# Kernel optimization log

Hardware: AMD Instinct MI355X
Metric: run time of the kernel (lower is better)

## Reference

```python
import jax, jax.numpy as jnp
import numpy as np

NUM_CODES = 100000
DIM = 64
N = 65536   # B*T flattened visits
L = 48      # max codes per visit (padded with -1)
C = 1.0     # Poincare ball curvature
MIN_NORM = 1e-15
BALL_EPS = 1e-5   # geoopt projx boundary eps for float32
ATANH_EPS = 1e-7  # clamp artanh argument below 1


def _projx(x):
    # Poincare ball projection: pull points with norm >= (1-eps)/sqrt(c) back inside.
    sqrt_c = jnp.sqrt(C)
    norm = jnp.maximum(jnp.linalg.norm(x, axis=-1, keepdims=True), MIN_NORM)
    maxnorm = (1.0 - BALL_EPS) / sqrt_c
    return jnp.where(norm > maxnorm, x * (maxnorm / norm), x)


def setup_inputs() -> dict:
    key = jax.random.key(0)
    k1, k2, k3 = jax.random.split(key, 3)
    emb = jax.random.normal(k1, (NUM_CODES, DIM), dtype=jnp.float32) * 0.001
    emb = _projx(emb)
    ids = jax.random.randint(k2, (N, L), 0, NUM_CODES)
    pad = jax.random.uniform(k3, (N, L)) < 0.3
    code_ids = jnp.where(pad, jnp.int64(-1) if jax.config.jax_enable_x64 else -1, ids)
    return {"code_ids": code_ids, "emb": emb}


def reference(code_ids, emb):
    # code_ids: [N, L] int, -1 = padding; emb: [NUM_CODES, DIM] Poincare points.
    sqrt_c = jnp.sqrt(jnp.asarray(C, emb.dtype))
    mask = code_ids >= 0                               # [N, L]
    safe_ids = jnp.where(mask, code_ids, 0)
    x = emb[safe_ids]                                  # [N, L, D] gather
    # logmap0: artanh(sqrt(c)*||x||) * x / (sqrt(c)*||x||)
    norm = jnp.maximum(jnp.linalg.norm(x, axis=-1, keepdims=True), MIN_NORM)
    arg = jnp.minimum(sqrt_c * norm, 1.0 - ATANH_EPS)
    tangents = (jnp.arctanh(arg) / (sqrt_c * norm)) * x  # [N, L, D]
    m = mask[..., None].astype(emb.dtype)
    s = jnp.sum(tangents * m, axis=1)                  # [N, D]
    cnt = jnp.sum(m, axis=1)                           # [N, 1]
    return s / jnp.maximum(cnt, 1.0)                   # zeros for empty visits
```

## Files before the change

### kernel.cpp

```cpp
#include <hip/hip_runtime.h>


#define LCODES 48
#define DIM 64

__global__ __launch_bounds__(256)
void amax_kernel(const float* __restrict__ emb, unsigned* __restrict__ bmax,
                 long n4) {
    const uint4* __restrict__ u4 = reinterpret_cast<const uint4*>(emb);
    unsigned m = 0;
    for (long i = (long)blockIdx.x * 256 + threadIdx.x; i < n4; i += 256L * 256L) {
        const uint4 w = u4[i];
        m = max(m, w.x & 0x7fffffffu);
        m = max(m, w.y & 0x7fffffffu);
        m = max(m, w.z & 0x7fffffffu);
        m = max(m, w.w & 0x7fffffffu);
    }
    #pragma unroll
    for (int d = 1; d <= 32; d <<= 1)
        m = max(m, (unsigned)__shfl_xor((int)m, d, 64));
    __shared__ unsigned sm[4];
    if ((threadIdx.x & 63) == 0) sm[threadIdx.x >> 6] = m;
    __syncthreads();
    if (threadIdx.x == 0)
        bmax[blockIdx.x] = max(max(sm[0], sm[1]), max(sm[2], sm[3]));
}

__device__ __forceinline__ float global_amax256(const unsigned* __restrict__ bmax) {
    const int lane = threadIdx.x & 63;
    unsigned m = max(max(bmax[lane], bmax[lane + 64]),
                     max(bmax[lane + 128], bmax[lane + 192]));
    #pragma unroll
    for (int d = 1; d <= 32; d <<= 1)
        m = max(m, (unsigned)__shfl_xor((int)m, d, 64));
    return __uint_as_float(m);
}

__global__ __launch_bounds__(256)
void build_i8_kernel(const float* __restrict__ emb,
                     const unsigned* __restrict__ bmax,
                     unsigned char* __restrict__ tab,
                     float* __restrict__ qsout, int C) {
    const float amax = global_amax256(bmax);
    const float qs   = amax * (1.0006f / 127.f);
    const float invq = (amax > 0.f) ? (127.f / (amax * 1.0006f)) : 0.f;
    if (blockIdx.x == 0 && threadIdx.x == 0) qsout[0] = qs;

    const int tid  = threadIdx.x;
    const int lane = tid & 63;
    const int wave = tid >> 6;
    const int g = lane >> 3, s = lane & 7;
    const int r = blockIdx.x * 32 + wave * 8 + g;
    if (r >= C) return;

    const float4* __restrict__ emb4 = reinterpret_cast<const float4*>(emb);
    const float4 a = emb4[r * 16 + 2 * s];
    const float4 b = emb4[r * 16 + 2 * s + 1];

    float ss = a.x*a.x + a.y*a.y + a.z*a.z + a.w*a.w
             + b.x*b.x + b.y*b.y + b.z*b.z + b.w*b.w;
    ss += __shfl_xor(ss, 1, 64);
    ss += __shfl_xor(ss, 2, 64);
    ss += __shfl_xor(ss, 4, 64);

    float scale;
    if (__builtin_expect(ss > 0.04f, 0)) {
        const float norm = fmaxf(sqrtf(ss), 1e-15f);
        const float arg  = fminf(norm, 1.f - 1e-7f);
        scale = 0.5f * logf((1.f + arg) / (1.f - arg)) / norm;
    } else {
        scale = 1.f + ss * (0.33333333333f + ss * (0.2f + ss * 0.14285714285f));
    }
    scale *= invq;

    const float t[8] = { a.x*scale, a.y*scale, a.z*scale, a.w*scale,
                         b.x*scale, b.y*scale, b.z*scale, b.w*scale };
    unsigned u[8];
    #pragma unroll
    for (int k = 0; k < 8; ++k)
        u[k] = (unsigned)((int)rintf(t[k]) + 128);

    uint2 w;
    w.x = u[0] | (u[1] << 8) | (u[2] << 16) | (u[3] << 24);
    w.y = u[4] | (u[5] << 8) | (u[6] << 16) | (u[7] << 24);
    reinterpret_cast<uint2*>(tab)[r * 8 + s] = w;
}

__global__ __launch_bounds__(256)
void visit_gather_i8x2_kernel(const int* __restrict__ ids,
                              const unsigned char* __restrict__ tab,
                              const float* __restrict__ qsp,
                              float* __restrict__ out, int N) {
    const float qs = qsp[0];

    const int tid  = threadIdx.x;
    const int lane = tid & 63;
    const int wave = tid >> 6;
    const int v0   = (blockIdx.x * 4 + wave) * 2;
    if (v0 >= N) return;
    const bool has1 = (v0 + 1) < N;

    int myid0 = -1, myid1 = -1;
    if (lane < LCODES) {
        myid0 = ids[(long)v0 * LCODES + lane];
        if (has1) myid1 = ids[(long)(v0 + 1) * LCODES + lane];
    }

    const float cnt0 = (float)__popcll(__ballot(myid0 >= 0));
    const float cnt1 = (float)__popcll(__ballot(myid1 >= 0));

    const int g = lane >> 3;
    const int s = lane & 7;
    const uint2* __restrict__ tab2 = reinterpret_cast<const uint2*>(tab);

    unsigned aEx0 = 0, aOx0 = 0, aEy0 = 0, aOy0 = 0;
    unsigned aEx1 = 0, aOx1 = 0, aEy1 = 0, aOy1 = 0;

    #pragma unroll
    for (int it = 0; it < LCODES / 8; ++it) {
        const int j   = it * 8 + g;
        const int id0 = __shfl(myid0, j, 64);
        const int id1 = __shfl(myid1, j, 64);
        const unsigned msk0  = (id0 >= 0) ? 0xffffffffu : 0u;
        const unsigned msk1  = (id1 >= 0) ? 0xffffffffu : 0u;
        const unsigned base0 = ((unsigned)(id0 >= 0 ? id0 : 0)) << 3;
        const unsigned base1 = ((unsigned)(id1 >= 0 ? id1 : 0)) << 3;

        uint2 w0 = tab2[base0 + s];
        uint2 w1 = tab2[base1 + s];
        w0.x &= msk0;  w0.y &= msk0;
        w1.x &= msk1;  w1.y &= msk1;

        aEx0 +=  w0.x       & 0x00ff00ffu;
        aOx0 += (w0.x >> 8) & 0x00ff00ffu;
        aEy0 +=  w0.y       & 0x00ff00ffu;
        aOy0 += (w0.y >> 8) & 0x00ff00ffu;
        aEx1 +=  w1.x       & 0x00ff00ffu;
        aOx1 += (w1.x >> 8) & 0x00ff00ffu;
        aEy1 +=  w1.y       & 0x00ff00ffu;
        aOy1 += (w1.y >> 8) & 0x00ff00ffu;
    }

    #pragma unroll
    for (int d = 8; d <= 32; d <<= 1) {
        aEx0 += (unsigned)__shfl_xor((int)aEx0, d, 64);
        aOx0 += (unsigned)__shfl_xor((int)aOx0, d, 64);
        aEy0 += (unsigned)__shfl_xor((int)aEy0, d, 64);
        aOy0 += (unsigned)__shfl_xor((int)aOy0, d, 64);
        aEx1 += (unsigned)__shfl_xor((int)aEx1, d, 64);
        aOx1 += (unsigned)__shfl_xor((int)aOx1, d, 64);
        aEy1 += (unsigned)__shfl_xor((int)aEy1, d, 64);
        aOy1 += (unsigned)__shfl_xor((int)aOy1, d, 64);
    }

    if (lane < 16) {
        const bool second = lane >= 8;
        if (!second || has1) {
            const int  ss8   = lane & 7;
            const int  v     = v0 + (second ? 1 : 0);
            const float cnt  = second ? cnt1 : cnt0;
            const unsigned eX = second ? aEx1 : aEx0;
            const unsigned oX = second ? aOx1 : aOx0;
            const unsigned eY = second ? aEy1 : aEy0;
            const unsigned oY = second ? aOy1 : aOy0;

            const float qinv  = qs / fmaxf(cnt, 1.f);
            const float fbias = 128.f * cnt;
            float4 rA, rB;
            rA.x = ((float)(eX & 0xffffu) - fbias) * qinv;
            rA.y = ((float)(oX & 0xffffu) - fbias) * qinv;
            rA.z = ((float)(eX >> 16)     - fbias) * qinv;
            rA.w = ((float)(oX >> 16)     - fbias) * qinv;
            rB.x = ((float)(eY & 0xffffu) - fbias) * qinv;
            rB.y = ((float)(oY & 0xffffu) - fbias) * qinv;
            rB.z = ((float)(eY >> 16)     - fbias) * qinv;
            rB.w = ((float)(oY >> 16)     - fbias) * qinv;
            float4* o = reinterpret_cast<float4*>(out) + (long)v * (DIM / 4);
            o[2 * ss8]     = rA;
            o[2 * ss8 + 1] = rB;
        }
    }
}

__global__ __launch_bounds__(256, 4)
void visit_fp32_kernel(const int* __restrict__ ids,
                       const float* __restrict__ emb,
                       float* __restrict__ out, int N) {
    const int tid  = threadIdx.x;
    const int lane = tid & 63;
    const int wave = tid >> 6;
    const int v    = blockIdx.x * 4 + wave;
    if (v >= N) return;

    int myid = -1;
    if (lane < LCODES) myid = ids[(long)v * LCODES + lane];
    const unsigned long long valid = __ballot(myid >= 0);
    const float cnt = (float)__popcll(valid);
    const int g = lane >> 3, s = lane & 7;
    const float4* __restrict__ emb4 = reinterpret_cast<const float4*>(emb);
    float4 accA = make_float4(0.f,0.f,0.f,0.f), accB = make_float4(0.f,0.f,0.f,0.f);
    #pragma unroll
    for (int it = 0; it < LCODES / 8; ++it) {
        const int id = __shfl(myid, it * 8 + g, 64);
        const float keep = (id >= 0) ? 1.f : 0.f;
        const unsigned base = ((unsigned)(id >= 0 ? id : 0)) << 4;
        float4 a = emb4[base + s], b = emb4[base + 8 + s];
        float ss = a.x*a.x + a.y*a.y + a.z*a.z + a.w*a.w
                 + b.x*b.x + b.y*b.y + b.z*b.z + b.w*b.w;
        ss += __shfl_xor(ss, 1, 64);
        ss += __shfl_xor(ss, 2, 64);
        ss += __shfl_xor(ss, 4, 64);
        float scale;
        if (__builtin_expect(__any(ss > 0.04f), 0)) {
            const float norm = fmaxf(sqrtf(ss), 1e-15f);
            const float arg  = fminf(norm, 1.f - 1e-7f);
            scale = 0.5f * logf((1.f + arg) / (1.f - arg)) / norm;
        } else {
            scale = 1.f + ss * (0.33333333333f + ss * (0.2f + ss * 0.14285714285f));
        }
        scale *= keep;
        accA.x += a.x*scale; accA.y += a.y*scale; accA.z += a.z*scale; accA.w += a.w*scale;
        accB.x += b.x*scale; accB.y += b.y*scale; accB.z += b.z*scale; accB.w += b.w*scale;
    }
    #pragma unroll
    for (int d = 8; d <= 32; d <<= 1) {
        accA.x += __shfl_xor(accA.x, d, 64); accA.y += __shfl_xor(accA.y, d, 64);
        accA.z += __shfl_xor(accA.z, d, 64); accA.w += __shfl_xor(accA.w, d, 64);
        accB.x += __shfl_xor(accB.x, d, 64); accB.y += __shfl_xor(accB.y, d, 64);
        accB.z += __shfl_xor(accB.z, d, 64); accB.w += __shfl_xor(accB.w, d, 64);
    }
    if (lane < 8) {
        const float inv = 1.f / fmaxf(cnt, 1.f);
        float4* o = reinterpret_cast<float4*>(out) + (long)v * (DIM / 4);
        o[2*s]   = make_float4(accA.x*inv, accA.y*inv, accA.z*inv, accA.w*inv);
        o[2*s+1] = make_float4(accB.x*inv, accB.y*inv, accB.z*inv, accB.w*inv);
    }
}

extern "C" void kernel_launch(void* const* d_in, const int* in_sizes, int n_in,
                              void* d_out, int out_size, void* d_ws, size_t ws_size,
                              hipStream_t stream) {
    const int*   ids = (const int*)d_in[0];
    const float* emb = (const float*)d_in[1];
    float*       out = (float*)d_out;

    const int N = in_sizes[0] / LCODES;
    const int C = in_sizes[1] / DIM;

    const size_t tab_off = 4096;
    const size_t need = tab_off + (size_t)C * DIM;

    if (ws_size >= need) {
        unsigned*      bmax = (unsigned*)d_ws;
        float*         qsp  = (float*)((char*)d_ws + 1024);
        unsigned char* tab  = (unsigned char*)d_ws + tab_off;

        const long n4 = (long)C * DIM / 4;
        hipLaunchKernelGGL(amax_kernel, dim3(256), dim3(256), 0, stream,
                           emb, bmax, n4);
        const int blocksA = (C + 31) / 32;
        hipLaunchKernelGGL(build_i8_kernel, dim3(blocksA), dim3(256), 0, stream,
                           emb, bmax, tab, qsp, C);
        const int blocksB = (N + 7) / 8;
        hipLaunchKernelGGL(visit_gather_i8x2_kernel, dim3(blocksB), dim3(256), 0,
                           stream, ids, tab, qsp, out, N);
    } else {
        const int blocks = (N + 3) / 4;
        hipLaunchKernelGGL(visit_fp32_kernel, dim3(blocks), dim3(256), 0, stream,
                           ids, emb, out, N);
    }
}
```

Baseline: 108.3 us.

## Widen int8 gather to 16-byte loads with zero-row padding and wider amax grid

The visit gather kernel now reads each table row as four 16-byte loads per code instead of eight 8-byte loads, handling 16 codes per iteration across the wave. Padding ids point to an extra all-zero row appended to the table, which removes the per-load masking. Index loads and output stores are marked nontemporal. The amax pre-pass uses 1024 blocks with two loads per iteration. The aim is fewer, wider memory transactions and more parallelism in the pre-pass, at the cost of more accumulator registers and a longer shuffle reduction.

Measured after the change: 112.8 us. 1.04x slower.

```diff
diff --git a/kernel.cpp b/kernel.cpp
--- a/kernel.cpp
+++ b/kernel.cpp
@@ -3,18 +3,28 @@
 
 #define LCODES 48
 #define DIM 64
+
+typedef float vf4 __attribute__((ext_vector_type(4)));
 
 __global__ __launch_bounds__(256)
 void amax_kernel(const float* __restrict__ emb, unsigned* __restrict__ bmax,
                  long n4) {
     const uint4* __restrict__ u4 = reinterpret_cast<const uint4*>(emb);
+    const long T = (long)gridDim.x * 256;
     unsigned m = 0;
-    for (long i = (long)blockIdx.x * 256 + threadIdx.x; i < n4; i += 256L * 256L) {
-        const uint4 w = u4[i];
-        m = max(m, w.x & 0x7fffffffu);
-        m = max(m, w.y & 0x7fffffffu);
-        m = max(m, w.z & 0x7fffffffu);
-        m = max(m, w.w & 0x7fffffffu);
+    for (long i = (long)blockIdx.x * 256 + threadIdx.x; i < n4; i += 2 * T) {
+        const uint4 a = u4[i];
+        m = max(m, a.x & 0x7fffffffu);
+        m = max(m, a.y & 0x7fffffffu);
+        m = max(m, a.z & 0x7fffffffu);
+        m = max(m, a.w & 0x7fffffffu);
+        if (i + T < n4) {
+            const uint4 b = u4[i + T];
+            m = max(m, b.x & 0x7fffffffu);
+            m = max(m, b.y & 0x7fffffffu);
+            m = max(m, b.z & 0x7fffffffu);
+            m = max(m, b.w & 0x7fffffffu);
+        }
     }
     #pragma unroll
     for (int d = 1; d <= 32; d <<= 1)
@@ -26,10 +36,12 @@
         bmax[blockIdx.x] = max(max(sm[0], sm[1]), max(sm[2], sm[3]));
 }
 
-__device__ __forceinline__ float global_amax256(const unsigned* __restrict__ bmax) {
+__device__ __forceinline__ float global_amax1024(const unsigned* __restrict__ bmax) {
     const int lane = threadIdx.x & 63;
-    unsigned m = max(max(bmax[lane], bmax[lane + 64]),
-                     max(bmax[lane + 128], bmax[lane + 192]));
+    unsigned m = 0;
+    #pragma unroll
+    for (int k = 0; k < 16; ++k)
+        m = max(m, bmax[lane + 64 * k]);
     #pragma unroll
     for (int d = 1; d <= 32; d <<= 1)
         m = max(m, (unsigned)__shfl_xor((int)m, d, 64));
@@ -41,10 +53,12 @@
                      const unsigned* __restrict__ bmax,
                      unsigned char* __restrict__ tab,
                      float* __restrict__ qsout, int C) {
-    const float amax = global_amax256(bmax);
+    const float amax = global_amax1024(bmax);
     const float qs   = amax * (1.0006f / 127.f);
     const float invq = (amax > 0.f) ? (127.f / (amax * 1.0006f)) : 0.f;
     if (blockIdx.x == 0 && threadIdx.x == 0) qsout[0] = qs;
+    if (blockIdx.x == 0 && threadIdx.x < 16)
+        reinterpret_cast<unsigned*>(tab + (size_t)C * DIM)[threadIdx.x] = 0u;
 
     const int tid  = threadIdx.x;
     const int lane = tid & 63;
@@ -87,10 +101,10 @@
 }
 
 __global__ __launch_bounds__(256)
-void visit_gather_i8x2_kernel(const int* __restrict__ ids,
+void visit_gather_i8x4_kernel(const int* __restrict__ ids,
                               const unsigned char* __restrict__ tab,
                               const float* __restrict__ qsp,
-                              float* __restrict__ out, int N) {
+                              float* __restrict__ out, int N, int C) {
     const float qs = qsp[0];
 
     const int tid  = threadIdx.x;
@@ -102,82 +116,81 @@
 
     int myid0 = -1, myid1 = -1;
     if (lane < LCODES) {
-        myid0 = ids[(long)v0 * LCODES + lane];
-        if (has1) myid1 = ids[(long)(v0 + 1) * LCODES + lane];
+        myid0 = __builtin_nontemporal_load(&ids[(long)v0 * LCODES + lane]);
+        if (has1)
+            myid1 = __builtin_nontemporal_load(&ids[(long)(v0 + 1) * LCODES + lane]);
     }
 
     const float cnt0 = (float)__popcll(__ballot(myid0 >= 0));
     const float cnt1 = (float)__popcll(__ballot(myid1 >= 0));
 
-    const int g = lane >> 3;
-    const int s = lane & 7;
-    const uint2* __restrict__ tab2 = reinterpret_cast<const uint2*>(tab);
-
-    unsigned aEx0 = 0, aOx0 = 0, aEy0 = 0, aOy0 = 0;
-    unsigned aEx1 = 0, aOx1 = 0, aEy1 = 0, aOy1 = 0;
-
-    #pragma unroll
-    for (int it = 0; it < LCODES / 8; ++it) {
-        const int j   = it * 8 + g;
+    const int g = lane >> 2;
+    const int s = lane & 3;
+    const uint4* __restrict__ tab4 = reinterpret_cast<const uint4*>(tab);
+
+    unsigned aE0[4] = {0,0,0,0}, aO0[4] = {0,0,0,0};
+    unsigned aE1[4] = {0,0,0,0}, aO1[4] = {0,0,0,0};
+
+    #pragma unroll
+    for (int it = 0; it < LCODES / 16; ++it) {
+        const int j   = it * 16 + g;
         const int id0 = __shfl(myid0, j, 64);
         const int id1 = __shfl(myid1, j, 64);
-        const unsigned msk0  = (id0 >= 0) ? 0xffffffffu : 0u;
-        const unsigned msk1  = (id1 >= 0) ? 0xffffffffu : 0u;
-        const unsigned base0 = ((unsigned)(id0 >= 0 ? id0 : 0)) << 3;
-        const unsigned base1 = ((unsigned)(id1 >= 0 ? id1 : 0)) << 3;
-
-        uint2 w0 = tab2[base0 + s];
-        uint2 w1 = tab2[base1 + s];
-        w0.x &= msk0;  w0.y &= msk0;
-        w1.x &= msk1;  w1.y &= msk1;
-
-        aEx0 +=  w0.x       & 0x00ff00ffu;
-        aOx0 += (w0.x >> 8) & 0x00ff00ffu;
-        aEy0 +=  w0.y       & 0x00ff00ffu;
-        aOy0 += (w0.y >> 8) & 0x00ff00ffu;
-        aEx1 +=  w1.x       & 0x00ff00ffu;
-        aOx1 += (w1.x >> 8) & 0x00ff00ffu;
-        aEy1 +=  w1.y       & 0x00ff00ffu;
-        aOy1 += (w1.y >> 8) & 0x00ff00ffu;
-    }
-
-    #pragma unroll
-    for (int d = 8; d <= 32; d <<= 1) {
-        aEx0 += (unsigned)__shfl_xor((int)aEx0, d, 64);
-        aOx0 += (unsigned)__shfl_xor((int)aOx0, d, 64);
-        aEy0 += (unsigned)__shfl_xor((int)aEy0, d, 64);
-        aOy0 += (unsigned)__shfl_xor((int)aOy0, d, 64);
-        aEx1 += (unsigned)__shfl_xor((int)aEx1, d, 64);
-        aOx1 += (unsigned)__shfl_xor((int)aOx1, d, 64);
-        aEy1 += (unsigned)__shfl_xor((int)aEy1, d, 64);
-        aOy1 += (unsigned)__shfl_xor((int)aOy1, d, 64);
-    }
-
-    if (lane < 16) {
-        const bool second = lane >= 8;
+        const unsigned b0 = ((unsigned)(id0 >= 0 ? id0 : C)) << 2;
+        const unsigned b1 = ((unsigned)(id1 >= 0 ? id1 : C)) << 2;
+
+        const uint4 w0 = tab4[b0 + s];
+        const uint4 w1 = tab4[b1 + s];
+
+        aE0[0] +=  w0.x       & 0x00ff00ffu;
+        aO0[0] += (w0.x >> 8) & 0x00ff00ffu;
+        aE0[1] +=  w0.y       & 0x00ff00ffu;
+        aO0[1] += (w0.y >> 8) & 0x00ff00ffu;
+        aE0[2] +=  w0.z       & 0x00ff00ffu;
+        aO0[2] += (w0.z >> 8) & 0x00ff00ffu;
+        aE0[3] +=  w0.w       & 0x00ff00ffu;
+        aO0[3] += (w0.w >> 8) & 0x00ff00ffu;
+        aE1[0] +=  w1.x       & 0x00ff00ffu;
+        aO1[0] += (w1.x >> 8) & 0x00ff00ffu;
+        aE1[1] +=  w1.y       & 0x00ff00ffu;
+        aO1[1] += (w1.y >> 8) & 0x00ff00ffu;
+        aE1[2] +=  w1.z       & 0x00ff00ffu;
+        aO1[2] += (w1.z >> 8) & 0x00ff00ffu;
+        aE1[3] +=  w1.w       & 0x00ff00ffu;
+        aO1[3] += (w1.w >> 8) & 0x00ff00ffu;
+    }
+
+    #pragma unroll
+    for (int d = 4; d <= 32; d <<= 1) {
+        #pragma unroll
+        for (int k = 0; k < 4; ++k) {
+            aE0[k] += (unsigned)__shfl_xor((int)aE0[k], d, 64);
+            aO0[k] += (unsigned)__shfl_xor((int)aO0[k], d, 64);
+            aE1[k] += (unsigned)__shfl_xor((int)aE1[k], d, 64);
+            aO1[k] += (unsigned)__shfl_xor((int)aO1[k], d, 64);
+        }
+    }
+
+    if (lane < 8) {
+        const bool second = lane >= 4;
         if (!second || has1) {
-            const int  ss8   = lane & 7;
-            const int  v     = v0 + (second ? 1 : 0);
-            const float cnt  = second ? cnt1 : cnt0;
-            const unsigned eX = second ? aEx1 : aEx0;
-            const unsigned oX = second ? aOx1 : aOx0;
-            const unsigned eY = second ? aEy1 : aEy0;
-            const unsigned oY = second ? aOy1 : aOy0;
-
+            const int   s4    = lane & 3;
+            const int   v     = v0 + (second ? 1 : 0);
+            const float cnt   = second ? cnt1 : cnt0;
             const float qinv  = qs / fmaxf(cnt, 1.f);
             const float fbias = 128.f * cnt;
-            float4 rA, rB;
-            rA.x = ((float)(eX & 0xffffu) - fbias) * qinv;
-            rA.y = ((float)(oX & 0xffffu) - fbias) * qinv;
-            rA.z = ((float)(eX >> 16)     - fbias) * qinv;
-            rA.w = ((float)(oX >> 16)     - fbias) * qinv;
-            rB.x = ((float)(eY & 0xffffu) - fbias) * qinv;
-            rB.y = ((float)(oY & 0xffffu) - fbias) * qinv;
-            rB.z = ((float)(eY >> 16)     - fbias) * qinv;
-            rB.w = ((float)(oY >> 16)     - fbias) * qinv;
-            float4* o = reinterpret_cast<float4*>(out) + (long)v * (DIM / 4);
-            o[2 * ss8]     = rA;
-            o[2 * ss8 + 1] = rB;
+            vf4* o = reinterpret_cast<vf4*>(out) + (long)v * (DIM / 4) + s4 * 4;
+            #pragma unroll
+            for (int k = 0; k < 4; ++k) {
+                const unsigned e = second ? aE1[k] : aE0[k];
+                const unsigned oo = second ? aO1[k] : aO0[k];
+                vf4 r;
+                r.x = ((float)(e  & 0xffffu) - fbias) * qinv;
+                r.y = ((float)(oo & 0xffffu) - fbias) * qinv;
+                r.z = ((float)(e  >> 16)     - fbias) * qinv;
+                r.w = ((float)(oo >> 16)     - fbias) * qinv;
+                __builtin_nontemporal_store(r, o + k);
+            }
         }
     }
 }
@@ -247,23 +260,23 @@
     const int N = in_sizes[0] / LCODES;
     const int C = in_sizes[1] / DIM;
 
-    const size_t tab_off = 4096;
-    const size_t need = tab_off + (size_t)C * DIM;
+    const size_t tab_off = 8192;
+    const size_t need = tab_off + (size_t)(C + 1) * DIM;
 
     if (ws_size >= need) {
         unsigned*      bmax = (unsigned*)d_ws;
-        float*         qsp  = (float*)((char*)d_ws + 1024);
+        float*         qsp  = (float*)((char*)d_ws + 4096);
         unsigned char* tab  = (unsigned char*)d_ws + tab_off;
 
         const long n4 = (long)C * DIM / 4;
-        hipLaunchKernelGGL(amax_kernel, dim3(256), dim3(256), 0, stream,
+        hipLaunchKernelGGL(amax_kernel, dim3(1024), dim3(256), 0, stream,
                            emb, bmax, n4);
         const int blocksA = (C + 31) / 32;
         hipLaunchKernelGGL(build_i8_kernel, dim3(blocksA), dim3(256), 0, stream,
                            emb, bmax, tab, qsp, C);
         const int blocksB = (N + 7) / 8;
-        hipLaunchKernelGGL(visit_gather_i8x2_kernel, dim3(blocksB), dim3(256), 0,
-                           stream, ids, tab, qsp, out, N);
+        hipLaunchKernelGGL(visit_gather_i8x4_kernel, dim3(blocksB), dim3(256), 0,
+                           stream, ids, tab, qsp, out, N, C);
     } else {
         const int blocks = (N + 3) / 4;
         hipLaunchKernelGGL(visit_fp32_kernel, dim3(blocks), dim3(256), 0, stream,
```
